# Kernel optimization log

Hardware: AMD Instinct MI355X
Metric: run time of the kernel (lower is better)

The kernel has to match this reference:

```python
import jax, jax.numpy as jnp
import numpy as np

N_GROUP = 64
GROUP_SIZE = 64
INPUT_DIM = 2048
BATCH = 8192
N_MONTN = 512


def setup_inputs() -> dict:
    key = jax.random.key(0)
    k1, k2, k3, k4, k5 = jax.random.split(key, 5)
    x = jax.random.normal(k1, (BATCH, INPUT_DIM), dtype=jnp.float32)
    weight = jax.random.normal(k2, (N_GROUP * GROUP_SIZE, INPUT_DIM), dtype=jnp.float32) * 0.02
    bias = jax.random.normal(k3, (N_GROUP * GROUP_SIZE,), dtype=jnp.float32) * 0.02
    rand_u = jax.random.uniform(k4, (BATCH,), dtype=jnp.float32)
    montn_index = jax.random.randint(k5, (N_MONTN,), 0, INPUT_DIM, dtype=jnp.int32)
    return {"x": x, "weight": weight, "bias": bias, "rand_u": rand_u,
            "montn_index": montn_index}


def reference(x, weight, bias, rand_u, montn_index):
    # Square the weights on monotone input columns (in-place in torch).
    w = weight.at[:, montn_index].set(weight[:, montn_index] ** 2)
    # y = x @ w^T + b  -> [B, n_group * n_group_size]
    y = jnp.einsum('bi,oi->bo', x, w) + bias
    B = y.shape[0]
    # per-group min over contiguous slices, then max over groups
    group_mins = y.reshape(B, N_GROUP, GROUP_SIZE).min(axis=2)  # [B, n_group]
    out = group_mins.max(axis=1)                                 # [B]
    # vectorized Bernoulli: 1.0 if u < sigmoid(out) else 0.0
    sample = (rand_u < jax.nn.sigmoid(out)).astype(jnp.float32)
    return sample.reshape(-1, 1)
```

## Files before the change

kernel.cpp:

```cpp
#include <hip/hip_runtime.h>
#include <cmath>


typedef _Float16 f16x8 __attribute__((ext_vector_type(8)));
typedef float f32x4 __attribute__((ext_vector_type(4)));

#define MARGIN_EPS 4e-3f
#define MAX_UNDEC 96

__device__ __forceinline__ void async_load16(const void* gptr, void* lptr) {
  __builtin_amdgcn_global_load_lds(
      (const __attribute__((address_space(1))) void*)gptr,
      (__attribute__((address_space(3))) void*)lptr, 16, 0, 0);
}

__device__ __forceinline__ float us2f(unsigned short u) {
  return (float)__builtin_bit_cast(_Float16, u);
}

__global__ void convert_split(float* __restrict__ x, float* __restrict__ wgt,
                              const int* __restrict__ montn,
                              int* __restrict__ count) {
  __shared__ unsigned msk[64];
  const int t = threadIdx.x, l = t & 63, w = t >> 6;
  const int r = blockIdx.x * 4 + w;
  const int use_mask = (r >= 8192) ? 1 : 0;
  if (blockIdx.x == 0 && t == 0) *count = 0;
  if (use_mask) {
    if (t < 64) msk[t] = 0u;
    __syncthreads();
    for (int j = t; j < 512; j += 256) {
      const int c = montn[j];
      atomicOr(&msk[c >> 5], 1u << (c & 31));
    }
    __syncthreads();
  }
  float* rowp = use_mask ? (wgt + (size_t)(r - 8192) * 2048)
                         : (x + (size_t)r * 2048);
  float4 v[4][2];
#pragma unroll
  for (int p = 0; p < 4; ++p) {
    v[p][0] = ((const float4*)rowp)[p * 128 + 2 * l];
    v[p][1] = ((const float4*)rowp)[p * 128 + 2 * l + 1];
  }
  unsigned mw[4];
#pragma unroll
  for (int p = 0; p < 4; ++p)
    mw[p] = use_mask ? msk[p * 16 + (l >> 2)] : 0u;

  unsigned short* up = (unsigned short*)rowp;
#pragma unroll
  for (int p = 0; p < 4; ++p) {
    float f[8];
    f[0] = v[p][0].x; f[1] = v[p][0].y; f[2] = v[p][0].z; f[3] = v[p][0].w;
    f[4] = v[p][1].x; f[5] = v[p][1].y; f[6] = v[p][1].z; f[7] = v[p][1].w;
    unsigned short hs[8], ls[8];
#pragma unroll
    for (int c = 0; c < 8; ++c) {
      float g = f[c];
      if ((mw[p] >> (8 * (l & 3) + c)) & 1u) g = g * g;
      _Float16 h = (_Float16)g;
      float res = g - (float)h;
      _Float16 lo = (_Float16)res;
      hs[c] = __builtin_bit_cast(unsigned short, h);
      ls[c] = __builtin_bit_cast(unsigned short, lo);
    }
    uint4 H, L;
    H.x = (unsigned)hs[0] | ((unsigned)hs[1] << 16);
    H.y = (unsigned)hs[2] | ((unsigned)hs[3] << 16);
    H.z = (unsigned)hs[4] | ((unsigned)hs[5] << 16);
    H.w = (unsigned)hs[6] | ((unsigned)hs[7] << 16);
    L.x = (unsigned)ls[0] | ((unsigned)ls[1] << 16);
    L.y = (unsigned)ls[2] | ((unsigned)ls[3] << 16);
    L.z = (unsigned)ls[4] | ((unsigned)ls[5] << 16);
    L.w = (unsigned)ls[6] | ((unsigned)ls[7] << 16);
    *((uint4*)(up + p * 512 + 8 * l)) = H;
    *((uint4*)(up + 2048 + p * 512 + 8 * l)) = L;
  }
}

__global__ __launch_bounds__(512, 2) void gemm_minmax(
    const unsigned short* __restrict__ X, const unsigned short* __restrict__ W,
    const float* __restrict__ bias, float* __restrict__ gmins) {
  __shared__ unsigned short As[2 * 256 * 64];
  __shared__ unsigned short Bs[2 * 256 * 64];
  const int t = threadIdx.x;
  const int lane = t & 63;
  const int w = t >> 6;
  const int wm = w >> 2;
  const int wn = w & 3;
  const int lin = blockIdx.x;
  const int m0 = (lin >> 4) * 256;
  const int n0 = (((lin & 7) << 1) + ((lin >> 3) & 1)) * 256;

  const int rowBase = w * 8 + (lane >> 3);
  const int gchunk = ((lane & 7) ^ ((lane >> 3) & 7)) * 8;
  const size_t gA0 = (size_t)(m0 + rowBase) * 4096 + gchunk;
  const size_t gB0 = (size_t)(n0 + rowBase) * 4096 + gchunk;
  const int w8row = w * 8;

  const int am = lane & 15, quad = lane >> 4;
  int arow[8], brw[4], swz[2];
#pragma unroll
  for (int i = 0; i < 8; ++i) arow[i] = (wm * 128 + i * 16 + am) * 64;
#pragma unroll
  for (int j = 0; j < 4; ++j) brw[j] = (wn * 64 + j * 16 + am) * 64;
#pragma unroll
  for (int h = 0; h < 2; ++h) swz[h] = (((h << 2) + quad) ^ (am & 7)) * 8;

  f32x4 acc[8][4];
#pragma unroll
  for (int i = 0; i < 8; ++i)
#pragma unroll
    for (int j = 0; j < 4; ++j) acc[i][j] = (f32x4){0.f, 0.f, 0.f, 0.f};

  auto STAGE_ALL = [&](int tile) {
    if (tile >= 32) return;
    const int bufo = (tile & 1) << 14;
    const size_t koff = (size_t)(tile << 6);
#pragma unroll
    for (int c = 0; c < 4; ++c)
      async_load16(X + gA0 + (size_t)(c * 64) * 4096 + koff,
                   As + bufo + (c * 64 + w8row) * 64);
#pragma unroll
    for (int c = 0; c < 4; ++c)
      async_load16(W + gB0 + (size_t)(c * 64) * 4096 + koff,
                   Bs + bufo + (c * 64 + w8row) * 64);
  };

  STAGE_ALL(0);
  __syncthreads();

#pragma unroll 2
  for (int kt = 0; kt < 32; ++kt) {
    const int bufo = (kt & 1) << 14;
    STAGE_ALL(kt + 1);
#pragma unroll
    for (int kk = 0; kk < 2; ++kk) {
      f16x8 av[8], bv[4];
#pragma unroll
      for (int i = 0; i < 8; ++i)
        av[i] = *(const f16x8*)(As + bufo + arow[i] + swz[kk]);
#pragma unroll
      for (int j = 0; j < 4; ++j)
        bv[j] = *(const f16x8*)(Bs + bufo + brw[j] + swz[kk]);
#pragma unroll
      for (int mb = 0; mb < 8; ++mb)
#pragma unroll
        for (int j = 0; j < 4; ++j)
          acc[mb][j] = __builtin_amdgcn_mfma_f32_16x16x32_f16(
              av[mb], bv[j], acc[mb][j], 0, 0, 0);
    }
    __syncthreads();
  }

  const int grp = (n0 >> 6) + wn;
  float bj[4];
#pragma unroll
  for (int j = 0; j < 4; ++j) bj[j] = bias[n0 + wn * 64 + j * 16 + am];
#pragma unroll
  for (int mb = 0; mb < 8; ++mb) {
#pragma unroll
    for (int reg = 0; reg < 4; ++reg) {
      float v = fminf(fminf(acc[mb][0][reg] + bj[0], acc[mb][1][reg] + bj[1]),
                      fminf(acc[mb][2][reg] + bj[2], acc[mb][3][reg] + bj[3]));
      v = fminf(v, __shfl_xor(v, 1, 64));
      v = fminf(v, __shfl_xor(v, 2, 64));
      v = fminf(v, __shfl_xor(v, 4, 64));
      v = fminf(v, __shfl_xor(v, 8, 64));
      if (am == 0) {
        const int row = m0 + wm * 128 + mb * 16 + quad * 4 + reg;
        gmins[(size_t)row * 64 + grp] = v;
      }
    }
  }
}

__global__ void finalize_margin(const float* __restrict__ gmins,
                                const float* __restrict__ rand_u,
                                float* __restrict__ out,
                                int* __restrict__ count, int* __restrict__ undec,
                                float4* __restrict__ ybuf4) {
  if (blockIdx.x < 384)
    ybuf4[(size_t)blockIdx.x * 256 + threadIdx.x] = (float4){0.f, 0.f, 0.f, 0.f};
  const int wv = threadIdx.x >> 6, lane = threadIdx.x & 63;
  const int row = blockIdx.x * 4 + wv;
  float v = gmins[(size_t)row * 64 + lane];
  v = fmaxf(v, __shfl_xor(v, 1, 64));
  v = fmaxf(v, __shfl_xor(v, 2, 64));
  v = fmaxf(v, __shfl_xor(v, 4, 64));
  v = fmaxf(v, __shfl_xor(v, 8, 64));
  v = fmaxf(v, __shfl_xor(v, 16, 64));
  v = fmaxf(v, __shfl_xor(v, 32, 64));
  if (lane == 0) {
    const float u = rand_u[row];
    const float slo = 1.0f / (1.0f + expf(-(v - MARGIN_EPS)));
    const float shi = 1.0f / (1.0f + expf(-(v + MARGIN_EPS)));
    if (u < slo) {
      out[row] = 1.0f;
    } else if (u >= shi) {
      out[row] = 0.0f;
    } else {
      const int i = atomicAdd(count, 1);
      if (i < 8192) undec[i] = row;
    }
  }
}

__global__ __launch_bounds__(256) void recompute_rows(
    const unsigned short* __restrict__ X, const unsigned short* __restrict__ W,
    const int* __restrict__ count, const int* __restrict__ undec,
    float* __restrict__ ybuf) {
  __shared__ float wf[64 * 129];
  __shared__ float part[256];
  const int g = blockIdx.x, kc = blockIdx.y;
  const int t = threadIdx.x;
  int n = *count;
  if (n > MAX_UNDEC) n = MAX_UNDEC;
  if (n == 0) return;

  {
    const int cl = t >> 2, ks = t & 3;
    const unsigned short* wp =
        W + (size_t)(g * 64 + cl) * 4096 + kc * 128 + ks * 32;
    float* dst = wf + cl * 129 + ks * 32;
#pragma unroll
    for (int i = 0; i < 32; i += 8) {
      uint4 hv = *(const uint4*)(wp + i);
      uint4 lv = *(const uint4*)(wp + 2048 + i);
      const unsigned* hw = (const unsigned*)&hv;
      const unsigned* lw = (const unsigned*)&lv;
#pragma unroll
      for (int m = 0; m < 4; ++m) {
        dst[i + 2 * m] = us2f((unsigned short)(hw[m] & 0xFFFF)) +
                         us2f((unsigned short)(lw[m] & 0xFFFF));
        dst[i + 2 * m + 1] = us2f((unsigned short)(hw[m] >> 16)) +
                             us2f((unsigned short)(lw[m] >> 16));
      }
    }
  }
  __syncthreads();

  const int col = t & 63, kq = t >> 6;
  const float* wcol = wf + col * 129 + kq * 32;
  for (int s = 0; s < n; ++s) {
    const int row = undec[s];
    const unsigned short* xp = X + (size_t)row * 4096 + kc * 128 + kq * 32;
    float acc = 0.f;
#pragma unroll
    for (int i = 0; i < 32; i += 8) {
      uint4 hv = *(const uint4*)(xp + i);
      uint4 lv = *(const uint4*)(xp + 2048 + i);
      const unsigned* hw = (const unsigned*)&hv;
      const unsigned* lw = (const unsigned*)&lv;
#pragma unroll
      for (int m = 0; m < 4; ++m) {
        const float x0 = us2f((unsigned short)(hw[m] & 0xFFFF)) +
                         us2f((unsigned short)(lw[m] & 0xFFFF));
        const float x1 = us2f((unsigned short)(hw[m] >> 16)) +
                         us2f((unsigned short)(lw[m] >> 16));
        acc = fmaf(x0, wcol[i + 2 * m], acc);
        acc = fmaf(x1, wcol[i + 2 * m + 1], acc);
      }
    }
    part[t] = acc;
    __syncthreads();
    if (t < 64) {
      const float y = part[t] + part[t + 64] + part[t + 128] + part[t + 192];
      atomicAdd(ybuf + (size_t)s * 4096 + g * 64 + t, y);
    }
    __syncthreads();
  }
}

__global__ void decide(const float* __restrict__ ybuf,
                       const int* __restrict__ undec, const int* __restrict__ count,
                       const float* __restrict__ bias,
                       const float* __restrict__ rand_u, float* __restrict__ out) {
  __shared__ float gm[64];
  int n = *count;
  if (n > MAX_UNDEC) n = MAX_UNDEC;
  const int s = blockIdx.x;
  if (s >= n) return;
  const int t = threadIdx.x;
  const int g = t >> 2, p4 = t & 3;
  const float* yb = ybuf + (size_t)s * 4096;
  const int c0 = g * 64 + p4 * 16;
  float m = 3.4e38f;
#pragma unroll
  for (int e = 0; e < 16; ++e) m = fminf(m, yb[c0 + e] + bias[c0 + e]);
  m = fminf(m, __shfl_xor(m, 1, 64));
  m = fminf(m, __shfl_xor(m, 2, 64));
  if (p4 == 0) gm[g] = m;
  __syncthreads();
  if (t < 64) {
    float v = gm[t];
    v = fmaxf(v, __shfl_xor(v, 1, 64));
    v = fmaxf(v, __shfl_xor(v, 2, 64));
    v = fmaxf(v, __shfl_xor(v, 4, 64));
    v = fmaxf(v, __shfl_xor(v, 8, 64));
    v = fmaxf(v, __shfl_xor(v, 16, 64));
    v = fmaxf(v, __shfl_xor(v, 32, 64));
    if (t == 0) {
      const int row = undec[s];
      const float sg = 1.0f / (1.0f + expf(-v));
      out[row] = (rand_u[row] < sg) ? 1.0f : 0.0f;
    }
  }
}

extern "C" void kernel_launch(void* const* d_in, const int* in_sizes, int n_in,
                              void* d_out, int out_size, void* d_ws, size_t ws_size,
                              hipStream_t stream) {
  float* x = (float*)d_in[0];
  float* weight = (float*)d_in[1];
  const float* bias = (const float*)d_in[2];
  const float* rand_u = (const float*)d_in[3];
  const int* montn = (const int*)d_in[4];
  float* out = (float*)d_out;

  char* ws = (char*)d_ws;
  int* count = (int*)ws;
  int* undec = (int*)(ws + 256);
  float* ybuf = (float*)(ws + 65536);
  float* gmins = (float*)(ws + 65536 + 1572864);

  convert_split<<<3072, 256, 0, stream>>>(x, weight, montn, count);
  gemm_minmax<<<512, 512, 0, stream>>>(
      (const unsigned short*)x, (const unsigned short*)weight, bias, gmins);
  finalize_margin<<<2048, 256, 0, stream>>>(gmins, rand_u, out, count, undec,
                                            (float4*)ybuf);
  recompute_rows<<<dim3(64, 16), 256, 0, stream>>>(
      (const unsigned short*)x, (const unsigned short*)weight, count, undec, ybuf);
  decide<<<MAX_UNDEC, 256, 0, stream>>>(ybuf, undec, count, bias, rand_u, out);
}
```

Baseline: 291.7 us.

## Switch GEMM main loop to 4-stage K=32 pipeline with explicit vmcnt waits

Replaces the double-buffered K=64 tile loop with a four-buffer ring of K=32 tiles, keeping three tiles of async global-to-LDS loads in flight. Each iteration waits on vmcnt and does a single barrier instead of the implicit full drain from __syncthreads. The aim is to hide global load latency better and cut barrier stalls. LDS footprint stays the same, but the loop runs twice as many iterations, each with half the MFMA work per barrier. The swizzle and address layout are recomputed for the narrower rows.

```diff
diff --git a/kernel.cpp b/kernel.cpp
--- a/kernel.cpp
+++ b/kernel.cpp
@@ -82,8 +82,8 @@
 __global__ __launch_bounds__(512, 2) void gemm_minmax(
     const unsigned short* __restrict__ X, const unsigned short* __restrict__ W,
     const float* __restrict__ bias, float* __restrict__ gmins) {
-  __shared__ unsigned short As[2 * 256 * 64];
-  __shared__ unsigned short Bs[2 * 256 * 64];
+  __shared__ unsigned short As[4 * 256 * 32];
+  __shared__ unsigned short Bs[4 * 256 * 32];
   const int t = threadIdx.x;
   const int lane = t & 63;
   const int w = t >> 6;
@@ -93,20 +93,20 @@
   const int m0 = (lin >> 4) * 256;
   const int n0 = (((lin & 7) << 1) + ((lin >> 3) & 1)) * 256;
 
-  const int rowBase = w * 8 + (lane >> 3);
-  const int gchunk = ((lane & 7) ^ ((lane >> 3) & 7)) * 8;
-  const size_t gA0 = (size_t)(m0 + rowBase) * 4096 + gchunk;
-  const size_t gB0 = (size_t)(n0 + rowBase) * 4096 + gchunk;
-  const int w8row = w * 8;
+  const int rowBase = w * 16 + (lane >> 2);
+  const int gch = ((lane & 3) ^ ((lane >> 3) & 3)) * 8;
+  const size_t gA0 = (size_t)(m0 + rowBase) * 4096 + gch;
+  const size_t gB0 = (size_t)(n0 + rowBase) * 4096 + gch;
+  unsigned short* ldsA = As + w * 512;
+  unsigned short* ldsB = Bs + w * 512;
 
   const int am = lane & 15, quad = lane >> 4;
-  int arow[8], brw[4], swz[2];
-#pragma unroll
-  for (int i = 0; i < 8; ++i) arow[i] = (wm * 128 + i * 16 + am) * 64;
-#pragma unroll
-  for (int j = 0; j < 4; ++j) brw[j] = (wn * 64 + j * 16 + am) * 64;
-#pragma unroll
-  for (int h = 0; h < 2; ++h) swz[h] = (((h << 2) + quad) ^ (am & 7)) * 8;
+  int arow[8], brw[4];
+#pragma unroll
+  for (int i = 0; i < 8; ++i) arow[i] = (wm * 128 + i * 16 + am) * 32;
+#pragma unroll
+  for (int j = 0; j < 4; ++j) brw[j] = (wn * 64 + j * 16 + am) * 32;
+  const int swz = (quad ^ ((lane >> 1) & 3)) * 8;
 
   f32x4 acc[8][4];
 #pragma unroll
@@ -114,45 +114,54 @@
 #pragma unroll
     for (int j = 0; j < 4; ++j) acc[i][j] = (f32x4){0.f, 0.f, 0.f, 0.f};
 
-  auto STAGE_ALL = [&](int tile) {
-    if (tile >= 32) return;
-    const int bufo = (tile & 1) << 14;
-    const size_t koff = (size_t)(tile << 6);
-#pragma unroll
-    for (int c = 0; c < 4; ++c)
-      async_load16(X + gA0 + (size_t)(c * 64) * 4096 + koff,
-                   As + bufo + (c * 64 + w8row) * 64);
-#pragma unroll
-    for (int c = 0; c < 4; ++c)
-      async_load16(W + gB0 + (size_t)(c * 64) * 4096 + koff,
-                   Bs + bufo + (c * 64 + w8row) * 64);
+  auto STAGE = [&](int tile) {
+    const int bufo = (tile & 3) << 13;
+    const size_t koff = (size_t)tile << 5;
+    async_load16(X + gA0 + koff, ldsA + bufo);
+    async_load16(X + gA0 + (size_t)128 * 4096 + koff, ldsA + bufo + 4096);
+    async_load16(W + gB0 + koff, ldsB + bufo);
+    async_load16(W + gB0 + (size_t)128 * 4096 + koff, ldsB + bufo + 4096);
   };
 
-  STAGE_ALL(0);
-  __syncthreads();
-
-#pragma unroll 2
-  for (int kt = 0; kt < 32; ++kt) {
-    const int bufo = (kt & 1) << 14;
-    STAGE_ALL(kt + 1);
-#pragma unroll
-    for (int kk = 0; kk < 2; ++kk) {
-      f16x8 av[8], bv[4];
-#pragma unroll
-      for (int i = 0; i < 8; ++i)
-        av[i] = *(const f16x8*)(As + bufo + arow[i] + swz[kk]);
-#pragma unroll
-      for (int j = 0; j < 4; ++j)
-        bv[j] = *(const f16x8*)(Bs + bufo + brw[j] + swz[kk]);
-#pragma unroll
-      for (int mb = 0; mb < 8; ++mb)
-#pragma unroll
-        for (int j = 0; j < 4; ++j)
-          acc[mb][j] = __builtin_amdgcn_mfma_f32_16x16x32_f16(
-              av[mb], bv[j], acc[mb][j], 0, 0, 0);
-    }
-    __syncthreads();
-  }
+  auto COMPUTE = [&](int kt) {
+    const int bufo = (kt & 3) << 13;
+    f16x8 av[8], bv[4];
+#pragma unroll
+    for (int i = 0; i < 8; ++i)
+      av[i] = *(const f16x8*)(As + bufo + arow[i] + swz);
+#pragma unroll
+    for (int j = 0; j < 4; ++j)
+      bv[j] = *(const f16x8*)(Bs + bufo + brw[j] + swz);
+#pragma unroll
+    for (int mb = 0; mb < 8; ++mb)
+#pragma unroll
+      for (int nb = 0; nb < 4; ++nb)
+        acc[mb][nb] = __builtin_amdgcn_mfma_f32_16x16x32_f16(
+            av[mb], bv[nb], acc[mb][nb], 0, 0, 0);
+  };
+
+  STAGE(0); STAGE(1); STAGE(2);
+
+#pragma unroll 1
+  for (int kt = 0; kt < 61; ++kt) {
+    asm volatile("s_waitcnt vmcnt(8)" ::: "memory");
+    __builtin_amdgcn_s_barrier();
+    __builtin_amdgcn_sched_barrier(0);
+    STAGE(kt + 3);
+    COMPUTE(kt);
+  }
+  asm volatile("s_waitcnt vmcnt(8)" ::: "memory");
+  __builtin_amdgcn_s_barrier();
+  __builtin_amdgcn_sched_barrier(0);
+  COMPUTE(61);
+  asm volatile("s_waitcnt vmcnt(4)" ::: "memory");
+  __builtin_amdgcn_s_barrier();
+  __builtin_amdgcn_sched_barrier(0);
+  COMPUTE(62);
+  asm volatile("s_waitcnt vmcnt(0)" ::: "memory");
+  __builtin_amdgcn_s_barrier();
+  __builtin_amdgcn_sched_barrier(0);
+  COMPUTE(63);
 
   const int grp = (n0 >> 6) + wn;
   float bj[4];
```

Measured after the change: 342.6 us. +17.4%, slower.
